# Kernel tuning notes

Measured on AMD Instinct MI355X. Metric: run time of the kernel, lower is better.

Reference implementation:

```python
import jax, jax.numpy as jnp
import numpy as np

B, N, L = 16, 128, 512            # batch, scan length, per-step feature (= configs.seq_len)
D, S, K, R, H = 1024, 16, 4, 64, 2048  # d_model, d_state, ker_size, dt_rank, hidden_dimention


def _mamba_params(key, scale=0.02):
    ks = jax.random.split(key, 6)
    return dict(
        in_w=jax.random.normal(ks[0], (2 * D, L)) * scale,
        conv_w=jax.random.normal(ks[1], (D, K)) * scale,
        conv_b=jnp.zeros((D,)),
        xproj_w=jax.random.normal(ks[2], (R + 2 * S, D)) * scale,
        dt_w=jax.random.normal(ks[3], (D, R)) * scale,
        dt_b=jax.random.normal(ks[4], (D,)) * scale,
        A_log=jnp.tile(jnp.log(jnp.arange(1, S + 1, dtype=jnp.float32)), (D, 1)),
        Dp=jnp.ones((D,)),
        out_w=jax.random.normal(ks[5], (L, D)) * scale,
    )


def setup_inputs():
    key = jax.random.key(0)
    kx, kf, kr, k1, k2 = jax.random.split(key, 5)
    inp = {"x": jax.random.normal(kx, (B, N, L), dtype=jnp.float32)}
    for pre, k in (("f_", kf), ("r_", kr)):
        for n, v in _mamba_params(k).items():
            inp[pre + n] = v
    inp["pu_w"] = jax.random.normal(k1, (H, L)) * 0.02
    inp["pu_b"] = jnp.zeros((H,))
    inp["pl_w"] = jax.random.normal(k2, (L, H)) * 0.02
    inp["pl_b"] = jnp.zeros((L,))
    inp["ln_g"] = jnp.ones((L,))
    inp["ln_b"] = jnp.zeros((L,))
    return inp


def _ln(x, g, b, eps=1e-5):
    m = x.mean(-1, keepdims=True)
    v = ((x - m) ** 2).mean(-1, keepdims=True)
    return (x - m) * jax.lax.rsqrt(v + eps) * g + b


def _dw_causal_conv(x, w, b):
    # x: [B,N,D]; depthwise causal conv along N with kernel [D,K]
    xt = jnp.pad(x.transpose(0, 2, 1), ((0, 0), (0, 0), (K - 1, 0)))  # [B,D,N+K-1]
    y = jax.lax.conv_general_dilated(xt, w[:, None, :], (1,), 'VALID',
                                     dimension_numbers=('NCH', 'OIH', 'NCH'),
                                     feature_group_count=D)
    return (y + b[None, :, None]).transpose(0, 2, 1)


def _mamba(x, in_w, conv_w, conv_b, xproj_w, dt_w, dt_b, A_log, Dp, out_w):
    # standard Mamba block (in_proj -> depthwise conv -> silu -> selective scan -> gate -> out_proj)
    xi, res = jnp.split(x @ in_w.T, 2, axis=-1)             # [B,N,D] each
    xc = jax.nn.silu(_dw_causal_conv(xi, conv_w, conv_b))   # [B,N,D]
    dbc = xc @ xproj_w.T                                    # [B,N,R+2S]
    dt, Bm, Cm = dbc[..., :R], dbc[..., R:R + S], dbc[..., R + S:]
    delta = jax.nn.softplus(dt @ dt_w.T + dt_b)             # [B,N,D]
    A = -jnp.exp(A_log)                                     # [D,S]
    dA = jnp.exp(delta[..., None] * A)                      # [B,N,D,S]
    dBx = delta[..., None] * Bm[:, :, None, :] * xc[..., None]

    def step(h, t):
        dA_t, dBx_t, C_t = t
        h = dA_t * h + dBx_t                                # [B,D,S]
        return h, jnp.einsum('bds,bs->bd', h, C_t)

    _, ys = jax.lax.scan(step, jnp.zeros((x.shape[0], D, S), x.dtype),
                         (dA.transpose(1, 0, 2, 3), dBx.transpose(1, 0, 2, 3), Cm.transpose(1, 0, 2)))
    y = ys.transpose(1, 0, 2) + xc * Dp                     # [B,N,D]
    y = y * jax.nn.silu(res)
    return y @ out_w.T                                      # [B,N,L]


def reference(x, f_in_w, f_conv_w, f_conv_b, f_xproj_w, f_dt_w, f_dt_b, f_A_log, f_Dp, f_out_w,
              r_in_w, r_conv_w, r_conv_b, r_xproj_w, r_dt_w, r_dt_b, r_A_log, r_Dp, r_out_w,
              pu_w, pu_b, pl_w, pl_b, ln_g, ln_b):
    y1 = _mamba(x, f_in_w, f_conv_w, f_conv_b, f_xproj_w, f_dt_w, f_dt_b, f_A_log, f_Dp, f_out_w)
    y2 = _mamba(x[:, ::-1, :], r_in_w, r_conv_w, r_conv_b, r_xproj_w, r_dt_w, r_dt_b, r_A_log, r_Dp, r_out_w)
    y3 = _ln(x + y1 + y2[:, ::-1, :], ln_g, ln_b)
    yp = jax.nn.relu(y3 @ pu_w.T + pu_b)
    yp = yp @ pl_w.T + pl_b
    return _ln(yp + y3, ln_g, ln_b)
```

## Files before the change

### kernel.cpp

```cpp
#include <hip/hip_runtime.h>
#include <hip/hip_bf16.h>
#include <cstdint>

typedef __hip_bfloat16 bf16;

constexpr int Bb = 16, Nn = 128, Ll = 512, Dd = 1024, Ss = 16, Rr = 64, Hh = 2048;
constexpr int Mm = Bb * Nn;
#define LOG2E 1.44269504088896340736f

using bf16x8 = __attribute__((ext_vector_type(8))) __bf16;
using bf16x4 = __attribute__((ext_vector_type(4))) __bf16;
using f32x4  = __attribute__((ext_vector_type(4))) float;

__device__ __forceinline__ float to_f(float x) { return x; }
__device__ __forceinline__ float to_f(bf16 x) { return __bfloat162float(x); }
__device__ __forceinline__ void store_t(float* p, float v) { *p = v; }
__device__ __forceinline__ void store_t(bf16* p, float v) { *p = __float2bfloat16(v); }
__device__ __forceinline__ __bf16 cvt1(float x) {
  bf16 h = __float2bfloat16(x);
  return *reinterpret_cast<__bf16*>(&h);
}
__device__ __forceinline__ float bfraw_to_f(__bf16 x) {
  bf16 h = *reinterpret_cast<bf16*>(&x);
  return __bfloat162float(h);
}
__device__ __forceinline__ bf16x8 load8(const bf16* p) { return *(const bf16x8*)p; }
__device__ __forceinline__ bf16x8 load8(const float* p) {
  float4 a = *(const float4*)p;
  float4 b = *(const float4*)(p + 4);
  bf16x8 r;
  r[0] = cvt1(a.x); r[1] = cvt1(a.y); r[2] = cvt1(a.z); r[3] = cvt1(a.w);
  r[4] = cvt1(b.x); r[5] = cvt1(b.y); r[6] = cvt1(b.z); r[7] = cvt1(b.w);
  return r;
}
__device__ __forceinline__ bf16x8 load8rt(const void* p, size_t idx, int isbf) {
  if (isbf) return load8((const bf16*)p + idx);
  return load8((const float*)p + idx);
}
__device__ __forceinline__ float ldf(const void* p, int i, int isbf) {
  if (isbf) return __bfloat162float(((const bf16*)p)[i]);
  return ((const float*)p)[i];
}

enum { EPI_STORE = 0, EPI_BIAS_RELU = 1, EPI_ADD = 3, EPI_BIAS = 4, EPI_BIAS_SOFTPLUS = 5,
       EPI_ATOMIC = 6 };

__global__ void sniff_kernel(const unsigned short* __restrict__ xs, int* __restrict__ flags) {
  const int tid = threadIdx.x;
  int cnt = 0;
  for (int j = 0; j < 64; ++j) {
    int i = tid + j * 256;
    unsigned short u = xs[(size_t)i * 64];
    bf16 h = *reinterpret_cast<bf16*>(&u);
    float v = __bfloat162float(h);
    float a = fabsf(v);
    if (v == 0.f || (a > 0.0009765625f && a < 16.f)) ++cnt;
  }
  __shared__ int sc[256];
  sc[tid] = cnt;
  __syncthreads();
  for (int o = 128; o > 0; o >>= 1) {
    if (tid < o) sc[tid] += sc[tid + o];
    __syncthreads();
  }
  if (tid == 0) flags[0] = (sc[0] > 8192) ? 1 : 0;
}

constexpr int LDT2 = 72;

template <typename TC, int EPI>
__global__ __launch_bounds__(256) void gemm_rt(
    const int* __restrict__ flagp,
    const void* __restrict__ A, int lda, int abf,
    const void* __restrict__ Bw, const void* __restrict__ Bw2, int ldb,
    int bmode, int bsplit,
    TC* __restrict__ C, int ldc,
    const void* __restrict__ bias, const void* __restrict__ bias2,
    int N, int Kchunk, int zk, size_t a_doff, size_t c_doff) {
  const int isbf = *flagp;
  const int ab = (abf == 2) ? isbf : abf;
  __shared__ __align__(16) __bf16 As[64 * LDT2];
  __shared__ __align__(16) __bf16 Bs[64 * LDT2];
  const int tid = threadIdx.x;
  const int wave = tid >> 6, lane = tid & 63;
  const int quad = lane >> 4, l16 = lane & 15;
  const int wm = wave & 1, wn = wave >> 1;
  int bx = blockIdx.x, by = blockIdx.y;
  const int gx = gridDim.x, gy = gridDim.y;
  if ((gx & 7) == 0) {
    int id = bx + gx * by;
    int xcd = id & 7, sl = id >> 3;
    by = sl % gy;
    bx = (sl / gy) * 8 + xcd;
  }
  int zsl = blockIdx.z;
  const void* Ap = A;
  const void* Bp0 = Bw;
  const void* biasp = bias;
  if (bmode == 3) {
    const int dir = zsl / zk;
    zsl = zsl % zk;
    if (dir) {
      Ap = (const char*)A + a_doff * (size_t)(ab ? 2 : 4);
      C += c_doff;
      Bp0 = Bw2;
      biasp = bias2;
    }
  }
  const int m0 = by * 64, n0 = bx * 64;
  const int kb = zsl * Kchunk;
  const int srow = tid >> 3;
  const int scol = (tid & 7) * 8;
  f32x4 acc[2][2] = {};
  for (int k0 = kb; k0 < kb + Kchunk; k0 += 64) {
#pragma unroll
    for (int h = 0; h < 2; ++h) {
      int r = srow + h * 32;
      *(bf16x8*)(&As[r * LDT2 + scol]) =
          load8rt(Ap, (size_t)(m0 + r) * lda + k0 + scol, ab);
      int rb = n0 + r;
      rb = rb < N ? rb : N - 1;
      const void* bp = Bp0;
      size_t bi;
      const int kk = k0 + scol;
      if (bmode == 1 && rb >= bsplit) {
        bp = Bw2; bi = (size_t)(rb - bsplit) * ldb + kk;
      } else if (bmode == 2 && kk >= bsplit) {
        bp = Bw2; bi = (size_t)rb * ldb + (kk - bsplit);
      } else {
        bi = (size_t)rb * ldb + kk;
      }
      *(bf16x8*)(&Bs[r * LDT2 + scol]) = load8rt(bp, bi, isbf);
    }
    __syncthreads();
#pragma unroll
    for (int kk2 = 0; kk2 < 2; ++kk2) {
      bf16x8 af[2], bfr[2];
#pragma unroll
      for (int i = 0; i < 2; ++i)
        af[i] = *(const bf16x8*)(&As[(wm * 32 + i * 16 + l16) * LDT2 + kk2 * 32 + quad * 8]);
#pragma unroll
      for (int j = 0; j < 2; ++j)
        bfr[j] = *(const bf16x8*)(&Bs[(wn * 32 + j * 16 + l16) * LDT2 + kk2 * 32 + quad * 8]);
#pragma unroll
      for (int i = 0; i < 2; ++i)
#pragma unroll
        for (int j = 0; j < 2; ++j)
          acc[i][j] = __builtin_amdgcn_mfma_f32_16x16x32_bf16(af[i], bfr[j], acc[i][j], 0, 0, 0);
    }
    __syncthreads();
  }
#pragma unroll
  for (int i = 0; i < 2; ++i) {
#pragma unroll
    for (int j = 0; j < 2; ++j) {
      const int col = n0 + wn * 32 + j * 16 + l16;
      if (col >= N) continue;
      float bv = 0.f;
      if (EPI == EPI_BIAS_RELU || EPI == EPI_BIAS || EPI == EPI_BIAS_SOFTPLUS)
        bv = ldf(biasp, col, isbf);
#pragma unroll
      for (int r = 0; r < 4; ++r) {
        const int row = m0 + wm * 32 + i * 16 + quad * 4 + r;
        size_t idx = (size_t)row * ldc + col;
        float v = acc[i][j][r];
        if (EPI == EPI_STORE) store_t(&C[idx], v);
        else if (EPI == EPI_BIAS_RELU) { v += bv; store_t(&C[idx], v > 0.f ? v : 0.f); }
        else if (EPI == EPI_BIAS) store_t(&C[idx], v + bv);
        else if (EPI == EPI_BIAS_SOFTPLUS) {
          v += bv;
          store_t(&C[idx], (v > 20.f) ? v : log1pf(__expf(v)));
        } else if (EPI == EPI_ATOMIC) {
          atomicAdd((float*)&C[idx], v);
        }
      }
    }
  }
}

__global__ __launch_bounds__(256) void zero_kernel(float4* __restrict__ p, int n4) {
  int i = blockIdx.x * 256 + threadIdx.x;
  if (i < n4) p[i] = float4{0.f, 0.f, 0.f, 0.f};
}

__global__ __launch_bounds__(256) void init_zbuf_rt(const int* __restrict__ flagp,
                                                    const void* __restrict__ x,
                                                    float* __restrict__ ZB) {
  const int isbf = *flagp;
  int i = blockIdx.x * 256 + threadIdx.x;
  float4 o;
  if (isbf) {
    ushort4 u = ((const ushort4*)x)[i];
    bf16 h0 = *reinterpret_cast<bf16*>(&u.x), h1 = *reinterpret_cast<bf16*>(&u.y);
    bf16 h2 = *reinterpret_cast<bf16*>(&u.z), h3 = *reinterpret_cast<bf16*>(&u.w);
    o = float4{__bfloat162float(h0), __bfloat162float(h1),
               __bfloat162float(h2), __bfloat162float(h3)};
  } else {
    o = ((const float4*)x)[i];
  }
  ((float4*)ZB)[i] = o;
}

__global__ __launch_bounds__(256) void conv_silu_rt(
    const int* __restrict__ flagp, const bf16* __restrict__ X2b,
    const void* __restrict__ fcw, const void* __restrict__ fcb,
    const void* __restrict__ rcw, const void* __restrict__ rcb,
    bf16* __restrict__ XCb) {
  const int isbf = *flagp;
  const int dir = blockIdx.y >> 2;
  const int d = (blockIdx.y & 3) * 256 + threadIdx.x;
  const int m = blockIdx.x;
  const int t = m & (Nn - 1);
  const void* cw = dir ? rcw : fcw;
  const void* cb = dir ? rcb : fcb;
  float w0 = ldf(cw, d * 4 + 0, isbf), w1 = ldf(cw, d * 4 + 1, isbf);
  float w2 = ldf(cw, d * 4 + 2, isbf), w3 = ldf(cw, d * 4 + 3, isbf);
  float a = ldf(cb, d, isbf);
  const size_t base = (size_t)m * 4096 + (size_t)dir * 2048 + d;
  if (dir == 0) {
    if (t >= 3) a += w0 * to_f(X2b[base - 3 * 4096]);
    if (t >= 2) a += w1 * to_f(X2b[base - 2 * 4096]);
    if (t >= 1) a += w2 * to_f(X2b[base - 1 * 4096]);
    a += w3 * to_f(X2b[base]);
  } else {
    if (t + 3 < Nn) a += w0 * to_f(X2b[base + 3 * 4096]);
    if (t + 2 < Nn) a += w1 * to_f(X2b[base + 2 * 4096]);
    if (t + 1 < Nn) a += w2 * to_f(X2b[base + 1 * 4096]);
    a += w3 * to_f(X2b[base]);
  }
  const float s = a / (1.f + __builtin_amdgcn_exp2f(-a * LOG2E));
  XCb[(size_t)m * 2048 + (size_t)dir * 1024 + d] = __float2bfloat16(s);
}

__global__ __launch_bounds__(256) void scan_gate2(
    const int* __restrict__ flagp,
    const float* __restrict__ DBC0, bf16* __restrict__ XCb, const bf16* __restrict__ X2b,
    const bf16* __restrict__ DELTA0,
    const void* __restrict__ fAlog, const void* __restrict__ fDp,
    const void* __restrict__ rAlog, const void* __restrict__ rDp) {
  const int isbf = *flagp;
  const int dir = blockIdx.z;
  const float* DBC = DBC0 + (size_t)dir * Mm * 96;
  const bf16* DELTA = DELTA0 + (size_t)dir * Mm * 1024;
  const void* A_log = dir ? rAlog : fAlog;
  const void* Dp = dir ? rDp : fDp;
  __shared__ __align__(16) __bf16 sBC[Nn * 32];
  __shared__ __align__(16) __bf16 sD[Nn * 16];
  __shared__ __align__(16) __bf16 sX[Nn * 16];
  __shared__ __align__(16) __bf16 sR[Nn * 16];
  __shared__ float sHend[4 * 16 * 16];
  __shared__ float sSdvEnd[4 * 16];
  const int b = blockIdx.x;
  const int d0 = blockIdx.y * 16;
  const int tid = threadIdx.x;
  const size_t rowbase = (size_t)b * Nn;
  const size_t xc_col = (size_t)dir * 1024;
#pragma unroll
  for (int k = 0; k < 16; ++k) {
    int idx = tid + k * 256;
    int t = idx >> 5, c = idx & 31;
    sBC[idx] = cvt1(DBC[(rowbase + t) * 96 + 64 + c]);
  }
  {
    int t = tid >> 1, h = tid & 1;
    *(uint4*)&sD[t * 16 + h * 8] = *(const uint4*)(DELTA + (rowbase + t) * 1024 + d0 + h * 8);
    *(uint4*)&sX[t * 16 + h * 8] =
        *(const uint4*)(XCb + (rowbase + t) * 2048 + xc_col + d0 + h * 8);
    *(uint4*)&sR[t * 16 + h * 8] =
        *(const uint4*)(X2b + (rowbase + t) * 4096 + (size_t)dir * 2048 + 1024 + d0 + h * 8);
  }
  __syncthreads();
  const int q = tid >> 6;
  const int lane = tid & 63;
  const int dl = lane & 15, sg = lane >> 4;
  const int d = d0 + dl;
  float A_[4];
#pragma unroll
  for (int j = 0; j < 4; ++j)
    A_[j] = -__expf(ldf(A_log, d * Ss + sg * 4 + j, isbf)) * LOG2E;
  float h0 = 0.f, h1 = 0.f, h2 = 0.f, h3 = 0.f, Sdv = 0.f;
  for (int j = 0; j < 32; ++j) {
    const int p = q * 32 + j;
    const int t = dir ? (Nn - 1 - p) : p;
    const float dv = bfraw_to_f(sD[t * 16 + dl]);
    const float xv = bfraw_to_f(sX[t * 16 + dl]);
    Sdv += dv;
    bf16x4 Bmv = *(const bf16x4*)&sBC[t * 32 + sg * 4];
    const float dx = dv * xv;
    h0 = __builtin_amdgcn_exp2f(dv * A_[0]) * h0 + dx * bfraw_to_f(Bmv[0]);
    h1 = __builtin_amdgcn_exp2f(dv * A_[1]) * h1 + dx * bfraw_to_f(Bmv[1]);
    h2 = __builtin_amdgcn_exp2f(dv * A_[2]) * h2 + dx * bfraw_to_f(Bmv[2]);
    h3 = __builtin_amdgcn_exp2f(dv * A_[3]) * h3 + dx * bfraw_to_f(Bmv[3]);
  }
  sHend[q * 256 + (sg * 4 + 0) * 16 + dl] = h0;
  sHend[q * 256 + (sg * 4 + 1) * 16 + dl] = h1;
  sHend[q * 256 + (sg * 4 + 2) * 16 + dl] = h2;
  sHend[q * 256 + (sg * 4 + 3) * 16 + dl] = h3;
  if (sg == 0) sSdvEnd[q * 16 + dl] = Sdv;
  __syncthreads();
  if (q == 0) {
    float r0 = 0.f, r1 = 0.f, r2 = 0.f, r3 = 0.f;
    for (int qq = 0; qq < 4; ++qq) {
      const float se = sSdvEnd[qq * 16 + dl];
      const float e0 = __builtin_amdgcn_exp2f(A_[0] * se);
      const float e1 = __builtin_amdgcn_exp2f(A_[1] * se);
      const float e2 = __builtin_amdgcn_exp2f(A_[2] * se);
      const float e3 = __builtin_amdgcn_exp2f(A_[3] * se);
      const int base = qq * 256 + sg * 4 * 16 + dl;
      float t0 = sHend[base + 0 * 16], t1 = sHend[base + 1 * 16];
      float t2 = sHend[base + 2 * 16], t3 = sHend[base + 3 * 16];
      sHend[base + 0 * 16] = r0; sHend[base + 1 * 16] = r1;
      sHend[base + 2 * 16] = r2; sHend[base + 3 * 16] = r3;
      r0 = e0 * r0 + t0; r1 = e1 * r1 + t1;
      r2 = e2 * r2 + t2; r3 = e3 * r3 + t3;
    }
  }
  __syncthreads();
  h0 = sHend[q * 256 + (sg * 4 + 0) * 16 + dl];
  h1 = sHend[q * 256 + (sg * 4 + 1) * 16 + dl];
  h2 = sHend[q * 256 + (sg * 4 + 2) * 16 + dl];
  h3 = sHend[q * 256 + (sg * 4 + 3) * 16 + dl];
  const float dp = ldf(Dp, d, isbf);
  for (int j = 0; j < 32; ++j) {
    const int p = q * 32 + j;
    const int t = dir ? (Nn - 1 - p) : p;
    const float dv = bfraw_to_f(sD[t * 16 + dl]);
    const float xv = bfraw_to_f(sX[t * 16 + dl]);
    bf16x4 Bmv = *(const bf16x4*)&sBC[t * 32 + sg * 4];
    bf16x4 Cmv = *(const bf16x4*)&sBC[t * 32 + 16 + sg * 4];
    const float dx = dv * xv;
    h0 = __builtin_amdgcn_exp2f(dv * A_[0]) * h0 + dx * bfraw_to_f(Bmv[0]);
    h1 = __builtin_amdgcn_exp2f(dv * A_[1]) * h1 + dx * bfraw_to_f(Bmv[1]);
    h2 = __builtin_amdgcn_exp2f(dv * A_[2]) * h2 + dx * bfraw_to_f(Bmv[2]);
    h3 = __builtin_amdgcn_exp2f(dv * A_[3]) * h3 + dx * bfraw_to_f(Bmv[3]);
    float acc = h0 * bfraw_to_f(Cmv[0]) + h1 * bfraw_to_f(Cmv[1]) +
                h2 * bfraw_to_f(Cmv[2]) + h3 * bfraw_to_f(Cmv[3]);
    acc += __shfl_xor(acc, 16, 64);
    acc += __shfl_xor(acc, 32, 64);
    if (sg == 0) {
      const float res = bfraw_to_f(sR[t * 16 + dl]);
      const float g = res / (1.f + __builtin_amdgcn_exp2f(-res * LOG2E));
      XCb[(rowbase + t) * 2048 + xc_col + d] = __float2bfloat16((acc + xv * dp) * g);
    }
  }
}

template <int MODE>
__global__ __launch_bounds__(256) void ln_rt(const int* __restrict__ flagp,
                                             const float* __restrict__ Z,
                                             const float* __restrict__ Zadd,
                                             const void* __restrict__ g,
                                             const void* __restrict__ bb,
                                             const void* __restrict__ pb,
                                             void* __restrict__ outp) {
  const int isbf = *flagp;
  const int row = blockIdx.x;
  const int tid = threadIdx.x;
  const int c0 = tid * 2;
  const float2* z = (const float2*)(Z + (size_t)row * Ll);
  float2 v = z[tid];
  if (MODE == 1) {
    const float2* za = (const float2*)(Zadd + (size_t)row * Ll);
    float2 a = za[tid];
    v.x += a.x + ldf(pb, c0, isbf);
    v.y += a.y + ldf(pb, c0 + 1, isbf);
  }
  float s = v.x + v.y, q = v.x * v.x + v.y * v.y;
#pragma unroll
  for (int o = 32; o > 0; o >>= 1) {
    s += __shfl_xor(s, o, 64);
    q += __shfl_xor(q, o, 64);
  }
  __shared__ float ss[4], qq[4];
  const int wv = tid >> 6, ln = tid & 63;
  if (ln == 0) { ss[wv] = s; qq[wv] = q; }
  __syncthreads();
  s = ss[0] + ss[1] + ss[2] + ss[3];
  q = qq[0] + qq[1] + qq[2] + qq[3];
  const float mean = s * (1.f / Ll);
  const float var = q * (1.f / Ll) - mean * mean;
  const float rs = rsqrtf(var + 1e-5f);
  const float o0 = (v.x - mean) * rs * ldf(g, c0, isbf) + ldf(bb, c0, isbf);
  const float o1 = (v.y - mean) * rs * ldf(g, c0 + 1, isbf) + ldf(bb, c0 + 1, isbf);
  if (MODE == 0) {
    float* out = (float*)outp;
    out[(size_t)row * Ll + c0] = o0;
    out[(size_t)row * Ll + c0 + 1] = o1;
  } else {
    if (isbf) {
      bf16* out = (bf16*)outp;
      out[(size_t)row * Ll + c0] = __float2bfloat16(o0);
      out[(size_t)row * Ll + c0 + 1] = __float2bfloat16(o1);
    } else {
      float* out = (float*)outp;
      out[(size_t)row * Ll + c0] = o0;
      out[(size_t)row * Ll + c0 + 1] = o1;
    }
  }
}

extern "C" void kernel_launch(void* const* d_in, const int* in_sizes, int n_in, void* d_out,
                              int out_size, void* d_ws, size_t ws_size, hipStream_t stream) {
  char* ws = (char*)d_ws;
  int* flags = (int*)ws;
  bf16* X2b = (bf16*)(ws + 256);
  bf16* XCb = X2b + (size_t)Mm * 4096;
  float* DBC = (float*)(XCb + (size_t)Mm * 2048);
  float* Z2 = DBC + (size_t)2 * Mm * 96;
  float* ZB = Z2 + (size_t)Mm * 512;
  float* Y3 = ZB + (size_t)Mm * 512;
  bf16* DELTA = (bf16*)(Y3 + (size_t)Mm * 512);
  bf16* H1 = X2b;
  size_t needed = 256 + 2 * ((size_t)Mm * 4096 + (size_t)Mm * 2048 + (size_t)2 * Mm * 1024) +
                  4 * ((size_t)2 * Mm * 96 + (size_t)3 * Mm * 512);
  if (ws_size < needed) return;

  const void* x = d_in[0];
  const dim3 blk(256);

  sniff_kernel<<<dim3(1), blk, 0, stream>>>((const unsigned short*)x, flags);
  init_zbuf_rt<<<dim3(Mm * Ll / 4 / 256), blk, 0, stream>>>(flags, x, ZB);
  zero_kernel<<<dim3((2 * Mm * 96 + Mm * 512) / 4 / 256), blk, 0, stream>>>(
      (float4*)DBC, (2 * Mm * 96 + Mm * 512) / 4);
  gemm_rt<bf16, EPI_STORE><<<dim3(64, 32), blk, 0, stream>>>(
      flags, x, Ll, 2, d_in[1], d_in[10], Ll, 1, 2048,
      X2b, 4096, nullptr, nullptr, 4096, Ll, 1, 0, 0);
  conv_silu_rt<<<dim3(Mm, 8), blk, 0, stream>>>(flags, X2b, d_in[2], d_in[3],
                                                d_in[11], d_in[12], XCb);
  gemm_rt<float, EPI_ATOMIC><<<dim3(2, 32, 8), blk, 0, stream>>>(
      flags, XCb, 2048, 1, d_in[4], d_in[13], Dd, 3, 0,
      DBC, 96, nullptr, nullptr, 96, 256, 4, 1024, (size_t)Mm * 96);
  gemm_rt<bf16, EPI_BIAS_SOFTPLUS><<<dim3(16, 32, 2), blk, 0, stream>>>(
      flags, DBC, 96, 0, d_in[5], d_in[14], Rr, 3, 0,
      DELTA, 1024, d_in[6], d_in[15], 1024, Rr, 1, (size_t)Mm * 96, (size_t)Mm * 1024);
  scan_gate2<<<dim3(Bb, Dd / 16, 2), blk, 0, stream>>>(
      flags, DBC, XCb, X2b, DELTA, d_in[7], d_in[8], d_in[16], d_in[17]);
  gemm_rt<float, EPI_ATOMIC><<<dim3(8, 32, 4), blk, 0, stream>>>(
      flags, XCb, 2048, 1, d_in[9], d_in[18], Dd, 2, 1024,
      ZB, Ll, nullptr, nullptr, Ll, 512, 1, 0, 0);
  ln_rt<0><<<dim3(Mm), blk, 0, stream>>>(flags, ZB, nullptr, d_in[23], d_in[24], nullptr, (void*)Y3);
  gemm_rt<bf16, EPI_BIAS_RELU><<<dim3(32, 32), blk, 0, stream>>>(
      flags, Y3, Ll, 0, d_in[19], nullptr, Ll, 0, 0,
      H1, Hh, d_in[20], nullptr, Hh, Ll, 1, 0, 0);
  gemm_rt<float, EPI_ATOMIC><<<dim3(8, 32, 2), blk, 0, stream>>>(
      flags, H1, Hh, 1, d_in[21], nullptr, Hh, 0, 0,
      Z2, Ll, nullptr, nullptr, Ll, 1024, 1, 0, 0);
  ln_rt<1><<<dim3(Mm), blk, 0, stream>>>(flags, Z2, Y3, d_in[23], d_in[24], d_in[22], d_out);

  (void)in_sizes; (void)n_in; (void)out_size;
}
```

Measured before the change: 358.4 us.

## Restructure selective scan to sequential per-thread, merge init kernels, emit bf16 LN output

```diff
diff --git a/kernel.cpp b/kernel.cpp
--- a/kernel.cpp
+++ b/kernel.cpp
@@ -178,27 +178,29 @@
   }
 }
 
-__global__ __launch_bounds__(256) void zero_kernel(float4* __restrict__ p, int n4) {
-  int i = blockIdx.x * 256 + threadIdx.x;
-  if (i < n4) p[i] = float4{0.f, 0.f, 0.f, 0.f};
-}
-
-__global__ __launch_bounds__(256) void init_zbuf_rt(const int* __restrict__ flagp,
-                                                    const void* __restrict__ x,
-                                                    float* __restrict__ ZB) {
+__global__ __launch_bounds__(256) void init_merge_rt(const int* __restrict__ flagp,
+                                                     const void* __restrict__ x,
+                                                     float* __restrict__ ZB,
+                                                     float* __restrict__ zerop,
+                                                     int nzb4, int nzero4) {
   const int isbf = *flagp;
   int i = blockIdx.x * 256 + threadIdx.x;
-  float4 o;
-  if (isbf) {
-    ushort4 u = ((const ushort4*)x)[i];
-    bf16 h0 = *reinterpret_cast<bf16*>(&u.x), h1 = *reinterpret_cast<bf16*>(&u.y);
-    bf16 h2 = *reinterpret_cast<bf16*>(&u.z), h3 = *reinterpret_cast<bf16*>(&u.w);
-    o = float4{__bfloat162float(h0), __bfloat162float(h1),
-               __bfloat162float(h2), __bfloat162float(h3)};
+  if (i < nzb4) {
+    float4 o;
+    if (isbf) {
+      ushort4 u = ((const ushort4*)x)[i];
+      bf16 h0 = *reinterpret_cast<bf16*>(&u.x), h1 = *reinterpret_cast<bf16*>(&u.y);
+      bf16 h2 = *reinterpret_cast<bf16*>(&u.z), h3 = *reinterpret_cast<bf16*>(&u.w);
+      o = float4{__bfloat162float(h0), __bfloat162float(h1),
+                 __bfloat162float(h2), __bfloat162float(h3)};
+    } else {
+      o = ((const float4*)x)[i];
+    }
+    ((float4*)ZB)[i] = o;
   } else {
-    o = ((const float4*)x)[i];
-  }
-  ((float4*)ZB)[i] = o;
+    int j = i - nzb4;
+    if (j < nzero4) ((float4*)zerop)[j] = float4{0.f, 0.f, 0.f, 0.f};
+  }
 }
 
 __global__ __launch_bounds__(256) void conv_silu_rt(
@@ -232,7 +234,7 @@
   XCb[(size_t)m * 2048 + (size_t)dir * 1024 + d] = __float2bfloat16(s);
 }
 
-__global__ __launch_bounds__(256) void scan_gate2(
+__global__ __launch_bounds__(128) void scan_gate3(
     const int* __restrict__ flagp,
     const float* __restrict__ DBC0, bf16* __restrict__ XCb, const bf16* __restrict__ X2b,
     const bf16* __restrict__ DELTA0,
@@ -245,101 +247,67 @@
   const void* A_log = dir ? rAlog : fAlog;
   const void* Dp = dir ? rDp : fDp;
   __shared__ __align__(16) __bf16 sBC[Nn * 32];
-  __shared__ __align__(16) __bf16 sD[Nn * 16];
-  __shared__ __align__(16) __bf16 sX[Nn * 16];
-  __shared__ __align__(16) __bf16 sR[Nn * 16];
-  __shared__ float sHend[4 * 16 * 16];
-  __shared__ float sSdvEnd[4 * 16];
+  __shared__ __align__(16) __bf16 sD[Nn * 32];
+  __shared__ __align__(16) __bf16 sX[Nn * 32];
+  __shared__ __align__(16) __bf16 sG[Nn * 32];
   const int b = blockIdx.x;
-  const int d0 = blockIdx.y * 16;
+  const int d0 = blockIdx.y * 32;
   const int tid = threadIdx.x;
   const size_t rowbase = (size_t)b * Nn;
   const size_t xc_col = (size_t)dir * 1024;
 #pragma unroll
-  for (int k = 0; k < 16; ++k) {
-    int idx = tid + k * 256;
-    int t = idx >> 5, c = idx & 31;
-    sBC[idx] = cvt1(DBC[(rowbase + t) * 96 + 64 + c]);
-  }
-  {
-    int t = tid >> 1, h = tid & 1;
-    *(uint4*)&sD[t * 16 + h * 8] = *(const uint4*)(DELTA + (rowbase + t) * 1024 + d0 + h * 8);
-    *(uint4*)&sX[t * 16 + h * 8] =
+  for (int k = 0; k < 8; ++k) {
+    int idx = tid + k * 128;
+    int t = idx >> 3, c = idx & 7;
+    float4 v = *(const float4*)(DBC + (rowbase + t) * 96 + 64 + c * 4);
+    bf16x4 pv = {cvt1(v.x), cvt1(v.y), cvt1(v.z), cvt1(v.w)};
+    int dst = (c < 4) ? (t * 32 + c * 8) : (t * 32 + (c - 4) * 8 + 4);
+    *(bf16x4*)&sBC[dst] = pv;
+  }
+#pragma unroll
+  for (int k = 0; k < 4; ++k) {
+    int idx = tid + k * 128;
+    int t = idx >> 2, h = idx & 3;
+    *(uint4*)&sD[t * 32 + h * 8] =
+        *(const uint4*)(DELTA + (rowbase + t) * 1024 + d0 + h * 8);
+    *(uint4*)&sX[t * 32 + h * 8] =
         *(const uint4*)(XCb + (rowbase + t) * 2048 + xc_col + d0 + h * 8);
-    *(uint4*)&sR[t * 16 + h * 8] =
-        *(const uint4*)(X2b + (rowbase + t) * 4096 + (size_t)dir * 2048 + 1024 + d0 + h * 8);
+    bf16x8 rv = *(const bf16x8*)(X2b + (rowbase + t) * 4096 + (size_t)dir * 2048 + 1024 + d0 + h * 8);
+    bf16x8 gv;
+#pragma unroll
+    for (int e = 0; e < 8; ++e) {
+      float r = bfraw_to_f(rv[e]);
+      gv[e] = cvt1(r / (1.f + __builtin_amdgcn_exp2f(-r * LOG2E)));
+    }
+    *(bf16x8*)&sG[t * 32 + h * 8] = gv;
   }
   __syncthreads();
-  const int q = tid >> 6;
-  const int lane = tid & 63;
+  const int wv = tid >> 6, lane = tid & 63;
   const int dl = lane & 15, sg = lane >> 4;
-  const int d = d0 + dl;
+  const int d_local = wv * 16 + dl;
+  const int d = d0 + d_local;
   float A_[4];
 #pragma unroll
   for (int j = 0; j < 4; ++j)
     A_[j] = -__expf(ldf(A_log, d * Ss + sg * 4 + j, isbf)) * LOG2E;
-  float h0 = 0.f, h1 = 0.f, h2 = 0.f, h3 = 0.f, Sdv = 0.f;
-  for (int j = 0; j < 32; ++j) {
-    const int p = q * 32 + j;
+  const float dp = ldf(Dp, d, isbf);
+  float h0 = 0.f, h1 = 0.f, h2 = 0.f, h3 = 0.f;
+  for (int p = 0; p < Nn; ++p) {
     const int t = dir ? (Nn - 1 - p) : p;
-    const float dv = bfraw_to_f(sD[t * 16 + dl]);
-    const float xv = bfraw_to_f(sX[t * 16 + dl]);
-    Sdv += dv;
-    bf16x4 Bmv = *(const bf16x4*)&sBC[t * 32 + sg * 4];
+    const float dv = bfraw_to_f(sD[t * 32 + d_local]);
+    const float xv = bfraw_to_f(sX[t * 32 + d_local]);
+    bf16x8 bc = *(const bf16x8*)&sBC[t * 32 + sg * 8];
     const float dx = dv * xv;
-    h0 = __builtin_amdgcn_exp2f(dv * A_[0]) * h0 + dx * bfraw_to_f(Bmv[0]);
-    h1 = __builtin_amdgcn_exp2f(dv * A_[1]) * h1 + dx * bfraw_to_f(Bmv[1]);
-    h2 = __builtin_amdgcn_exp2f(dv * A_[2]) * h2 + dx * bfraw_to_f(Bmv[2]);
-    h3 = __builtin_amdgcn_exp2f(dv * A_[3]) * h3 + dx * bfraw_to_f(Bmv[3]);
-  }
-  sHend[q * 256 + (sg * 4 + 0) * 16 + dl] = h0;
-  sHend[q * 256 + (sg * 4 + 1) * 16 + dl] = h1;
-  sHend[q * 256 + (sg * 4 + 2) * 16 + dl] = h2;
-  sHend[q * 256 + (sg * 4 + 3) * 16 + dl] = h3;
-  if (sg == 0) sSdvEnd[q * 16 + dl] = Sdv;
-  __syncthreads();
-  if (q == 0) {
-    float r0 = 0.f, r1 = 0.f, r2 = 0.f, r3 = 0.f;
-    for (int qq = 0; qq < 4; ++qq) {
-      const float se = sSdvEnd[qq * 16 + dl];
-      const float e0 = __builtin_amdgcn_exp2f(A_[0] * se);
-      const float e1 = __builtin_amdgcn_exp2f(A_[1] * se);
-      const float e2 = __builtin_amdgcn_exp2f(A_[2] * se);
-      const float e3 = __builtin_amdgcn_exp2f(A_[3] * se);
-      const int base = qq * 256 + sg * 4 * 16 + dl;
-      float t0 = sHend[base + 0 * 16], t1 = sHend[base + 1 * 16];
-      float t2 = sHend[base + 2 * 16], t3 = sHend[base + 3 * 16];
-      sHend[base + 0 * 16] = r0; sHend[base + 1 * 16] = r1;
-      sHend[base + 2 * 16] = r2; sHend[base + 3 * 16] = r3;
-      r0 = e0 * r0 + t0; r1 = e1 * r1 + t1;
-      r2 = e2 * r2 + t2; r3 = e3 * r3 + t3;
-    }
-  }
-  __syncthreads();
-  h0 = sHend[q * 256 + (sg * 4 + 0) * 16 + dl];
-  h1 = sHend[q * 256 + (sg * 4 + 1) * 16 + dl];
-  h2 = sHend[q * 256 + (sg * 4 + 2) * 16 + dl];
-  h3 = sHend[q * 256 + (sg * 4 + 3) * 16 + dl];
-  const float dp = ldf(Dp, d, isbf);
-  for (int j = 0; j < 32; ++j) {
-    const int p = q * 32 + j;
-    const int t = dir ? (Nn - 1 - p) : p;
-    const float dv = bfraw_to_f(sD[t * 16 + dl]);
-    const float xv = bfraw_to_f(sX[t * 16 + dl]);
-    bf16x4 Bmv = *(const bf16x4*)&sBC[t * 32 + sg * 4];
-    bf16x4 Cmv = *(const bf16x4*)&sBC[t * 32 + 16 + sg * 4];
-    const float dx = dv * xv;
-    h0 = __builtin_amdgcn_exp2f(dv * A_[0]) * h0 + dx * bfraw_to_f(Bmv[0]);
-    h1 = __builtin_amdgcn_exp2f(dv * A_[1]) * h1 + dx * bfraw_to_f(Bmv[1]);
-    h2 = __builtin_amdgcn_exp2f(dv * A_[2]) * h2 + dx * bfraw_to_f(Bmv[2]);
-    h3 = __builtin_amdgcn_exp2f(dv * A_[3]) * h3 + dx * bfraw_to_f(Bmv[3]);
-    float acc = h0 * bfraw_to_f(Cmv[0]) + h1 * bfraw_to_f(Cmv[1]) +
-                h2 * bfraw_to_f(Cmv[2]) + h3 * bfraw_to_f(Cmv[3]);
+    h0 = __builtin_amdgcn_exp2f(dv * A_[0]) * h0 + dx * bfraw_to_f(bc[0]);
+    h1 = __builtin_amdgcn_exp2f(dv * A_[1]) * h1 + dx * bfraw_to_f(bc[1]);
+    h2 = __builtin_amdgcn_exp2f(dv * A_[2]) * h2 + dx * bfraw_to_f(bc[2]);
+    h3 = __builtin_amdgcn_exp2f(dv * A_[3]) * h3 + dx * bfraw_to_f(bc[3]);
+    float acc = h0 * bfraw_to_f(bc[4]) + h1 * bfraw_to_f(bc[5]) +
+                h2 * bfraw_to_f(bc[6]) + h3 * bfraw_to_f(bc[7]);
     acc += __shfl_xor(acc, 16, 64);
     acc += __shfl_xor(acc, 32, 64);
     if (sg == 0) {
-      const float res = bfraw_to_f(sR[t * 16 + dl]);
-      const float g = res / (1.f + __builtin_amdgcn_exp2f(-res * LOG2E));
+      const float g = bfraw_to_f(sG[t * 32 + d_local]);
       XCb[(rowbase + t) * 2048 + xc_col + d] = __float2bfloat16((acc + xv * dp) * g);
     }
   }
@@ -352,7 +320,8 @@
                                              const void* __restrict__ g,
                                              const void* __restrict__ bb,
                                              const void* __restrict__ pb,
-                                             void* __restrict__ outp) {
+                                             void* __restrict__ outp,
+                                             bf16* __restrict__ outp2) {
   const int isbf = *flagp;
   const int row = blockIdx.x;
   const int tid = threadIdx.x;
@@ -386,6 +355,8 @@
     float* out = (float*)outp;
     out[(size_t)row * Ll + c0] = o0;
     out[(size_t)row * Ll + c0 + 1] = o1;
+    outp2[(size_t)row * Ll + c0] = __float2bfloat16(o0);
+    outp2[(size_t)row * Ll + c0 + 1] = __float2bfloat16(o1);
   } else {
     if (isbf) {
       bf16* out = (bf16*)outp;
@@ -409,19 +380,23 @@
   float* Z2 = DBC + (size_t)2 * Mm * 96;
   float* ZB = Z2 + (size_t)Mm * 512;
   float* Y3 = ZB + (size_t)Mm * 512;
-  bf16* DELTA = (bf16*)(Y3 + (size_t)Mm * 512);
+  bf16* Y3b = (bf16*)(Y3 + (size_t)Mm * 512);
+  bf16* DELTA = Y3b + (size_t)Mm * 512;
   bf16* H1 = X2b;
-  size_t needed = 256 + 2 * ((size_t)Mm * 4096 + (size_t)Mm * 2048 + (size_t)2 * Mm * 1024) +
+  size_t needed = 256 +
+                  2 * ((size_t)Mm * 4096 + (size_t)Mm * 2048 + (size_t)Mm * 512 +
+                       (size_t)2 * Mm * 1024) +
                   4 * ((size_t)2 * Mm * 96 + (size_t)3 * Mm * 512);
   if (ws_size < needed) return;
 
   const void* x = d_in[0];
   const dim3 blk(256);
+  const int nzb4 = Mm * Ll / 4;
+  const int nzero4 = (2 * Mm * 96 + Mm * 512) / 4;
 
   sniff_kernel<<<dim3(1), blk, 0, stream>>>((const unsigned short*)x, flags);
-  init_zbuf_rt<<<dim3(Mm * Ll / 4 / 256), blk, 0, stream>>>(flags, x, ZB);
-  zero_kernel<<<dim3((2 * Mm * 96 + Mm * 512) / 4 / 256), blk, 0, stream>>>(
-      (float4*)DBC, (2 * Mm * 96 + Mm * 512) / 4);
+  init_merge_rt<<<dim3((nzb4 + nzero4 + 255) / 256), blk, 0, stream>>>(
+      flags, x, ZB, DBC, nzb4, nzero4);
   gemm_rt<bf16, EPI_STORE><<<dim3(64, 32), blk, 0, stream>>>(
       flags, x, Ll, 2, d_in[1], d_in[10], Ll, 1, 2048,
       X2b, 4096, nullptr, nullptr, 4096, Ll, 1, 0, 0);
@@ -433,19 +408,21 @@
   gemm_rt<bf16, EPI_BIAS_SOFTPLUS><<<dim3(16, 32, 2), blk, 0, stream>>>(
       flags, DBC, 96, 0, d_in[5], d_in[14], Rr, 3, 0,
       DELTA, 1024, d_in[6], d_in[15], 1024, Rr, 1, (size_t)Mm * 96, (size_t)Mm * 1024);
-  scan_gate2<<<dim3(Bb, Dd / 16, 2), blk, 0, stream>>>(
+  scan_gate3<<<dim3(Bb, Dd / 32, 2), dim3(128), 0, stream>>>(
       flags, DBC, XCb, X2b, DELTA, d_in[7], d_in[8], d_in[16], d_in[17]);
   gemm_rt<float, EPI_ATOMIC><<<dim3(8, 32, 4), blk, 0, stream>>>(
       flags, XCb, 2048, 1, d_in[9], d_in[18], Dd, 2, 1024,
       ZB, Ll, nullptr, nullptr, Ll, 512, 1, 0, 0);
-  ln_rt<0><<<dim3(Mm), blk, 0, stream>>>(flags, ZB, nullptr, d_in[23], d_in[24], nullptr, (void*)Y3);
+  ln_rt<0><<<dim3(Mm), blk, 0, stream>>>(flags, ZB, nullptr, d_in[23], d_in[24], nullptr,
+                                         (void*)Y3, Y3b);
   gemm_rt<bf16, EPI_BIAS_RELU><<<dim3(32, 32), blk, 0, stream>>>(
-      flags, Y3, Ll, 0, d_in[19], nullptr, Ll, 0, 0,
+      flags, Y3b, Ll, 1, d_in[19], nullptr, Ll, 0, 0,
       H1, Hh, d_in[20], nullptr, Hh, Ll, 1, 0, 0);
   gemm_rt<float, EPI_ATOMIC><<<dim3(8, 32, 2), blk, 0, stream>>>(
       flags, H1, Hh, 1, d_in[21], nullptr, Hh, 0, 0,
       Z2, Ll, nullptr, nullptr, Ll, 1024, 1, 0, 0);
-  ln_rt<1><<<dim3(Mm), blk, 0, stream>>>(flags, Z2, Y3, d_in[23], d_in[24], d_in[22], d_out);
+  ln_rt<1><<<dim3(Mm), blk, 0, stream>>>(flags, Z2, Y3, d_in[23], d_in[24], d_in[22],
+                                         d_out, nullptr);
 
   (void)in_sizes; (void)n_in; (void)out_size;
 }
```

New measurement: 352.2 us. No clear change (-1.7%).
